# Kernel optimization log

Measured on AMD Instinct MI355X. Metric: run time of the kernel, lower is better.

The kernel has to match this reference:

```python
import jax, jax.numpy as jnp
import numpy as np

L2_REG = 0.02
EPS = 1e-8  # torch F.cosine_similarity eps


def setup_inputs() -> dict:
    key = jax.random.key(0)
    N, d = 8192, 512
    examples = jax.random.normal(key, (N, 2, d), dtype=jnp.float32)
    return {"examples": examples}


def reference(examples):
    # examples: (N, 2, d)
    anchors = examples[:, 0, :]    # (N, d)
    positives = examples[:, 1, :]  # (N, d)

    a_norm = jnp.linalg.norm(anchors, axis=-1)    # (N,)
    p_norm = jnp.linalg.norm(positives, axis=-1)  # (N,)

    # positive similarity: cos(a_i, p_i), torch-style eps clamp on norm product
    pos_sim = jnp.sum(anchors * positives, axis=-1) / jnp.maximum(a_norm * p_norm, EPS)  # (N,)

    # full cosine similarity matrix S[i, j] = cos(a_i, p_j) via normalized GEMM
    dots = jnp.einsum('id,jd->ij', anchors, positives)  # (N, N)
    denom = jnp.maximum(a_norm[:, None] * p_norm[None, :], EPS)
    neg_sim = dots / denom

    # diagonal of negatives is replaced by the anchor itself: cos(a_i, a_i)
    diag_val = (a_norm * a_norm) / jnp.maximum(a_norm * a_norm, EPS)  # ~1.0, eps-faithful
    N = anchors.shape[0]
    idx = jnp.arange(N)
    neg_sim = neg_sim.at[idx, idx].set(diag_val)

    logits = jnp.concatenate([pos_sim[:, None], neg_sim], axis=1)  # (N, N+1)
    # cross-entropy with labels all zero -> -log_softmax(...)[:, 0], mean over N
    ce = -jnp.mean(jax.nn.log_softmax(logits, axis=-1)[:, 0])

    l2_term = L2_REG * jnp.linalg.norm(examples)  # Frobenius norm of full input
    return ce + l2_term
```

## Files before the change

kernel.cpp:

```cpp
#include <hip/hip_runtime.h>
#include <hip/hip_bf16.h>


#define NR 8192
#define DD 512
#define E_CONST 2.71828182845904523536f

typedef __attribute__((ext_vector_type(4))) float f32x4_t;
typedef __attribute__((ext_vector_type(4))) int   i32x4_t;
typedef __attribute__((ext_vector_type(8))) int   i32x8_t;
typedef unsigned char uchar;
typedef unsigned int  uint;
#define AS1 __attribute__((address_space(1)))
#define AS3 __attribute__((address_space(3)))

__global__ __launch_bounds__(128) void prep_kernel(
    const float* __restrict__ ex,
    uchar* __restrict__ Ah, uchar* __restrict__ Ph,
    float* __restrict__ pos_sim, float* __restrict__ norm2,
    float* __restrict__ rowsum)
{
    const int i = blockIdx.x;
    const int t = threadIdx.x;
    const float4 a = ((const float4*)(ex + (size_t)i * 1024))[t];
    const float4 p = ((const float4*)(ex + (size_t)i * 1024 + 512))[t];
    float sa  = a.x*a.x + a.y*a.y + a.z*a.z + a.w*a.w;
    float sp  = p.x*p.x + p.y*p.y + p.z*p.z + p.w*p.w;
    float sap = a.x*p.x + a.y*p.y + a.z*p.z + a.w*p.w;
    #pragma unroll
    for (int m = 1; m < 64; m <<= 1) {
        sa  += __shfl_xor(sa,  m, 64);
        sp  += __shfl_xor(sp,  m, 64);
        sap += __shfl_xor(sap, m, 64);
    }
    __shared__ float red[3][2];
    if ((t & 63) == 0) { red[0][t>>6] = sa; red[1][t>>6] = sp; red[2][t>>6] = sap; }
    __syncthreads();
    sa  = red[0][0] + red[0][1];
    sp  = red[1][0] + red[1][1];
    sap = red[2][0] + red[2][1];
    const float inva = rsqrtf(sa);
    const float invp = rsqrtf(sp);
    uint pa = 0, pp = 0;
    pa = __builtin_amdgcn_cvt_pk_fp8_f32(a.x * inva, a.y * inva, pa, false);
    pa = __builtin_amdgcn_cvt_pk_fp8_f32(a.z * inva, a.w * inva, pa, true);
    pp = __builtin_amdgcn_cvt_pk_fp8_f32(p.x * invp, p.y * invp, pp, false);
    pp = __builtin_amdgcn_cvt_pk_fp8_f32(p.z * invp, p.w * invp, pp, true);
    ((uint*)Ah)[i * 128 + t] = pa;
    ((uint*)Ph)[i * 128 + t] = pp;
    if (t == 0) {
        pos_sim[i] = sap * inva * invp;
        norm2[i]   = sa + sp;
        rowsum[i]  = 0.0f;
    }
}

__global__ __launch_bounds__(256, 2) void gemm_kernel(
    const uchar* __restrict__ Ah, const uchar* __restrict__ Ph,
    float* __restrict__ rowsum)
{
    __shared__ uchar ls[65536];
    const int t  = threadIdx.x;
    const int w  = t >> 6;
    const int l  = t & 63;
    const int wr = w >> 1, wc = w & 1;
    const int ll = l & 15, lh = l >> 4;
    const int m0 = blockIdx.y * 128;
    const int n0 = blockIdx.x * 128;

    f32x4_t acc[4][4];
    #pragma unroll
    for (int i = 0; i < 4; i++)
        #pragma unroll
        for (int j = 0; j < 4; j++)
            acc[i][j] = (f32x4_t){0.f, 0.f, 0.f, 0.f};

    auto stage = [&](const uchar* src, int s, int matOff, int rowBase) {
        const int buf = s & 1;
        #pragma unroll
        for (int j = 0; j < 4; ++j) {
            const int r  = w * 32 + j * 8 + (l >> 3);
            const int gs = (l & 7) ^ (r & 7);
            const uchar* g = src + (size_t)(rowBase + r) * DD + s * 128 + gs * 16;
            __builtin_amdgcn_global_load_lds(
                (const AS1 void*)g,
                (AS3 void*)(&ls[buf * 32768 + matOff + w * 4096 + j * 1024 + l * 16]),
                16, 0, 0);
        }
    };

    auto rdfrag = [&](int base, int R) -> i32x8_t {
        const int rb = base + R * 128;
        i32x4_t lo = *(const i32x4_t*)&ls[rb + (((lh * 2)    ) ^ (ll & 7)) * 16];
        i32x4_t hi = *(const i32x4_t*)&ls[rb + (((lh * 2) + 1) ^ (ll & 7)) * 16];
        return __builtin_shufflevector(lo, hi, 0, 1, 2, 3, 4, 5, 6, 7);
    };

    stage(Ah, 0, 0,     m0);
    stage(Ph, 0, 16384, n0);
    __syncthreads();

    #pragma unroll
    for (int s = 0; s < 4; ++s) {
        if (s < 3) {
            stage(Ah, s + 1, 0,     m0);
            stage(Ph, s + 1, 16384, n0);
        }
        const int aB = (s & 1) * 32768;
        const int bB = aB + 16384;

        i32x8_t bf[4];
        #pragma unroll
        for (int ni = 0; ni < 4; ++ni)
            bf[ni] = rdfrag(bB, wc * 64 + ni * 16 + ll);

        #pragma unroll
        for (int mi = 0; mi < 4; ++mi) {
            i32x8_t af = rdfrag(aB, wr * 64 + mi * 16 + ll);
            __builtin_amdgcn_s_setprio(1);
            #pragma unroll
            for (int ni = 0; ni < 4; ++ni)
                acc[mi][ni] =
                    __builtin_amdgcn_mfma_scale_f32_16x16x128_f8f6f4(
                        af, bf[ni], acc[mi][ni],
                        0, 0,
                        0, 0x7F7F7F7F,
                        0, 0x7F7F7F7F);
            __builtin_amdgcn_s_setprio(0);
        }
        __syncthreads();
    }

    #pragma unroll
    for (int mi = 0; mi < 4; ++mi) {
        #pragma unroll
        for (int r = 0; r < 4; ++r) {
            float s = __expf(acc[mi][0][r]) + __expf(acc[mi][1][r]) +
                      __expf(acc[mi][2][r]) + __expf(acc[mi][3][r]);
            s += __shfl_xor(s, 1, 64);
            s += __shfl_xor(s, 2, 64);
            s += __shfl_xor(s, 4, 64);
            s += __shfl_xor(s, 8, 64);
            if (ll == 0)
                atomicAdd(&rowsum[m0 + wr * 64 + mi * 16 + lh * 4 + r], s);
        }
    }
}

__global__ __launch_bounds__(1024) void final_kernel(
    const float* __restrict__ rowsum, const float* __restrict__ pos_sim,
    const float* __restrict__ norm2, float* __restrict__ out)
{
    const int t = threadIdx.x;
    float s1 = 0.f, s2 = 0.f;
    #pragma unroll
    for (int k = 0; k < NR / 1024; ++k) {
        const int i = k * 1024 + t;
        s1 += logf(rowsum[i] + E_CONST) - pos_sim[i];
        s2 += norm2[i];
    }
    #pragma unroll
    for (int m = 1; m < 64; m <<= 1) {
        s1 += __shfl_xor(s1, m, 64);
        s2 += __shfl_xor(s2, m, 64);
    }
    __shared__ float r1[16], r2[16];
    if ((t & 63) == 0) { r1[t >> 6] = s1; r2[t >> 6] = s2; }
    __syncthreads();
    if (t == 0) {
        float a = 0.f, b = 0.f;
        #pragma unroll
        for (int k = 0; k < 16; ++k) { a += r1[k]; b += r2[k]; }
        out[0] = a * (1.0f / NR) + 0.02f * sqrtf(b);
    }
}

extern "C" void kernel_launch(void* const* d_in, const int* in_sizes, int n_in,
                              void* d_out, int out_size, void* d_ws, size_t ws_size,
                              hipStream_t stream) {
    const float* ex = (const float*)d_in[0];
    float* out = (float*)d_out;
    char* ws = (char*)d_ws;
    uchar* Ah      = (uchar*)(ws);
    uchar* Ph      = (uchar*)(ws + 4194304);
    float* possim  = (float*)(ws + 8388608);
    float* norm2   = (float*)(ws + 8388608 + 32768);
    float* rowsum  = (float*)(ws + 8388608 + 65536);

    prep_kernel<<<NR, 128, 0, stream>>>(ex, Ah, Ph, possim, norm2, rowsum);
    gemm_kernel<<<dim3(NR / 128, NR / 128), 256, 0, stream>>>(Ah, Ph, rowsum);
    final_kernel<<<1, 1024, 0, stream>>>(rowsum, possim, norm2, out);
}
```

Baseline: 183.9 us.

## Load GEMM fragments directly from global memory, dropping LDS staging

The GEMM kernel no longer stages A and P tiles into double-buffered shared memory through global_load_lds. Each lane now reads its MFMA fragments straight from global memory, which removes the 64KB of LDS and all block barriers. The launch-bounds occupancy hint rises from 2 to 4 blocks per CU. The cost is that tiles shared between waves are re-fetched from global memory or L2 rather than reused from LDS, and the 32-byte per-lane loads have a row stride of 512 bytes, so access is less coalesced.

```diff
diff --git a/kernel.cpp b/kernel.cpp
--- a/kernel.cpp
+++ b/kernel.cpp
@@ -11,8 +11,6 @@
 typedef __attribute__((ext_vector_type(8))) int   i32x8_t;
 typedef unsigned char uchar;
 typedef unsigned int  uint;
-#define AS1 __attribute__((address_space(1)))
-#define AS3 __attribute__((address_space(3)))
 
 __global__ __launch_bounds__(128) void prep_kernel(
     const float* __restrict__ ex,
@@ -55,11 +53,10 @@
     }
 }
 
-__global__ __launch_bounds__(256, 2) void gemm_kernel(
+__global__ __launch_bounds__(256, 4) void gemm_kernel(
     const uchar* __restrict__ Ah, const uchar* __restrict__ Ph,
     float* __restrict__ rowsum)
 {
-    __shared__ uchar ls[65536];
     const int t  = threadIdx.x;
     const int w  = t >> 6;
     const int l  = t & 63;
@@ -75,48 +72,25 @@
         for (int j = 0; j < 4; j++)
             acc[i][j] = (f32x4_t){0.f, 0.f, 0.f, 0.f};
 
-    auto stage = [&](const uchar* src, int s, int matOff, int rowBase) {
-        const int buf = s & 1;
-        #pragma unroll
-        for (int j = 0; j < 4; ++j) {
-            const int r  = w * 32 + j * 8 + (l >> 3);
-            const int gs = (l & 7) ^ (r & 7);
-            const uchar* g = src + (size_t)(rowBase + r) * DD + s * 128 + gs * 16;
-            __builtin_amdgcn_global_load_lds(
-                (const AS1 void*)g,
-                (AS3 void*)(&ls[buf * 32768 + matOff + w * 4096 + j * 1024 + l * 16]),
-                16, 0, 0);
-        }
-    };
-
-    auto rdfrag = [&](int base, int R) -> i32x8_t {
-        const int rb = base + R * 128;
-        i32x4_t lo = *(const i32x4_t*)&ls[rb + (((lh * 2)    ) ^ (ll & 7)) * 16];
-        i32x4_t hi = *(const i32x4_t*)&ls[rb + (((lh * 2) + 1) ^ (ll & 7)) * 16];
-        return __builtin_shufflevector(lo, hi, 0, 1, 2, 3, 4, 5, 6, 7);
-    };
-
-    stage(Ah, 0, 0,     m0);
-    stage(Ph, 0, 16384, n0);
-    __syncthreads();
+    const uchar* Abase = Ah + (size_t)(m0 + wr * 64 + ll) * DD + lh * 32;
+    const uchar* Bbase = Ph + (size_t)(n0 + wc * 64 + ll) * DD + lh * 32;
 
     #pragma unroll
     for (int s = 0; s < 4; ++s) {
-        if (s < 3) {
-            stage(Ah, s + 1, 0,     m0);
-            stage(Ph, s + 1, 16384, n0);
-        }
-        const int aB = (s & 1) * 32768;
-        const int bB = aB + 16384;
-
         i32x8_t bf[4];
         #pragma unroll
-        for (int ni = 0; ni < 4; ++ni)
-            bf[ni] = rdfrag(bB, wc * 64 + ni * 16 + ll);
-
+        for (int ni = 0; ni < 4; ++ni) {
+            const uchar* p = Bbase + ni * 16 * DD + s * 128;
+            i32x4_t lo = *(const i32x4_t*)p;
+            i32x4_t hi = *(const i32x4_t*)(p + 16);
+            bf[ni] = __builtin_shufflevector(lo, hi, 0, 1, 2, 3, 4, 5, 6, 7);
+        }
         #pragma unroll
         for (int mi = 0; mi < 4; ++mi) {
-            i32x8_t af = rdfrag(aB, wr * 64 + mi * 16 + ll);
+            const uchar* p = Abase + mi * 16 * DD + s * 128;
+            i32x4_t lo = *(const i32x4_t*)p;
+            i32x4_t hi = *(const i32x4_t*)(p + 16);
+            i32x8_t af = __builtin_shufflevector(lo, hi, 0, 1, 2, 3, 4, 5, 6, 7);
             __builtin_amdgcn_s_setprio(1);
             #pragma unroll
             for (int ni = 0; ni < 4; ++ni)
@@ -128,7 +102,6 @@
                         0, 0x7F7F7F7F);
             __builtin_amdgcn_s_setprio(0);
         }
-        __syncthreads();
     }
 
     #pragma unroll
```

Measured after the change: 394.5 us. 2.15x slower.
